# Kernel tuning notes

Measured on AMD Instinct MI355X. Metric: run time of the kernel, lower is better.

Reference implementation:

```python
import jax, jax.numpy as jnp
import numpy as np

N, D, YD, L = 500000, 256, 50, 1000


def setup_inputs() -> dict:
    key = jax.random.key(0)
    k_x, k_l, k_y, k_w1, k_w2 = jax.random.split(key, 5)
    lim1 = 1.0 / np.sqrt(D)
    return {
        "x": jax.random.normal(k_x, (N, D), dtype=jnp.float32),
        "labels": jax.random.randint(k_l, (N,), 0, L, dtype=jnp.int32),
        "y": jax.random.uniform(k_y, (N, YD), dtype=jnp.float32),
        "w1": jax.random.uniform(k_w1, (D, 1), jnp.float32, -lim1, lim1),
        "b1": jnp.zeros((1,), jnp.float32),
        "w2": jax.random.uniform(k_w2, (D, YD), jnp.float32, -lim1, lim1),
        "b2": jnp.zeros((YD,), jnp.float32),
        "num_labels": L,
    }


def reference(x, labels, y, w1, b1, w2, b2, num_labels):
    # sigmoid-gated features: a = sigmoid(x @ w1 + b1) * x   [N, D]
    a = jax.nn.sigmoid(x @ w1 + b1) * x
    # segment counts per label (labels assumed dense 0..L-1, all present)
    counts = jax.ops.segment_sum(jnp.ones((x.shape[0],), x.dtype), labels,
                                 num_segments=num_labels)
    denom = jnp.maximum(counts, 1.0)[:, None]  # guard empty segments
    # segment mean of gated features  [L, D]
    res = jax.ops.segment_sum(a, labels, num_segments=num_labels) / denom
    # softmax(linear2(res))  [L, YD]
    prediction = jax.nn.softmax(res @ w2 + b2, axis=1)
    # segment mean of soft targets  [L, YD]
    y_mean = jax.ops.segment_sum(y, labels, num_segments=num_labels) / denom
    # torch CrossEntropyLoss with probability targets applies log_softmax
    # to its input (here: already-softmaxed prediction) -- faithful double softmax
    logp = jax.nn.log_softmax(prediction, axis=1)
    return -jnp.mean(jnp.sum(y_mean * logp, axis=1))
```

## Files before the change

kernel.cpp:

```cpp
#include <hip/hip_runtime.h>
#include <math.h>

#define NROWS 500000
#define DIM 256
#define YDIM 50
#define NLAB 1000

#define XT 64
#define NTX ((NROWS + XT - 1) / XT)
#define XBLOCKS 256
#define ASTRIDE 264
#define ZC 51

#define YT 128
#define NTY ((NROWS + YT - 1) / YT)
#define YBLOCKS 256

typedef __attribute__((ext_vector_type(8))) short frag_ab;
typedef __attribute__((ext_vector_type(4))) float frag_cd;

__device__ __forceinline__ float b2f(unsigned short u) {
    return __uint_as_float(((unsigned)u) << 16);
}
__device__ __forceinline__ unsigned short f2b(float f) {
    unsigned u = __float_as_uint(f);
    return (unsigned short)((u + 0x7fffu + ((u >> 16) & 1u)) >> 16);
}
__device__ __forceinline__ unsigned cvt_pk_bf16(float lo, float hi) {
    unsigned r;
    asm("v_cvt_pk_bf16_f32 %0, %1, %2" : "=v"(r) : "v"(lo), "v"(hi));
    return r;
}
__device__ __forceinline__ void bar_lds() {
    asm volatile("s_waitcnt lgkmcnt(0)\n\ts_barrier" ::: "memory");
}

__global__ __launch_bounds__(1024) void k_xstream(
    const float* __restrict__ x, const int* __restrict__ labels,
    const float* __restrict__ w1, const float* __restrict__ b1,
    const float* __restrict__ w2, unsigned short* __restrict__ zpart,
    float* __restrict__ out)
{
    __shared__ __align__(16) unsigned short sA[XT * ASTRIDE];
    __shared__ __align__(16) float zst[XT][52];
    __shared__ __align__(16) unsigned short accz[NLAB * YDIM];
    __shared__ int slab[2][XT];

    const int tid = threadIdx.x, lane = tid & 63, wib = tid >> 6;
    const int bid = blockIdx.x;
    const int mh = wib >> 2, jt = wib & 3;

    if (bid == 0 && tid == 0) out[0] = 0.0f;
    for (int k = tid; k < NLAB * YDIM / 2; k += 1024)
        reinterpret_cast<unsigned*>(accz)[k] = 0u;

    frag_ab bfr[8];
    {
        const int n = 16 * jt + (lane & 15);
        #pragma unroll
        for (int s = 0; s < 8; ++s) {
            const int k0 = 32 * s + (lane >> 4) * 8;
            #pragma unroll
            for (int i = 0; i < 8; ++i) {
                const int kk = k0 + i;
                float v = 0.f;
                if (n < YDIM)       v = w2[kk * YDIM + n];
                else if (n == YDIM) v = w1[kk];
                bfr[s][i] = (short)f2b(v);
            }
        }
    }
    const float b1v = b1[0];
    __syncthreads();

    auto PREF = [&](int t, float4* r) {
        #pragma unroll
        for (int k = 0; k < 4; ++k) {
            const int rg = t * XT + 4 * wib + k;
            r[k] = (rg < NROWS)
                 ? reinterpret_cast<const float4*>(x)[(size_t)rg * 64 + lane]
                 : make_float4(0.f, 0.f, 0.f, 0.f);
        }
    };
    auto LLAB = [&](int t) -> int {
        const int rg = t * XT + tid;
        return (tid < XT && rg < NROWS) ? labels[rg] : 0;
    };

    auto process = [&](int pft, float4* r, int& lb, int par) {
        if (tid < XT) slab[par][tid] = lb;
        uint2 pk[4];
        #pragma unroll
        for (int k = 0; k < 4; ++k) {
            pk[k].x = cvt_pk_bf16(r[k].x, r[k].y);
            pk[k].y = cvt_pk_bf16(r[k].z, r[k].w);
        }
        PREF(pft, r);
        lb = LLAB(pft);
        const int row = 4 * wib;
        #pragma unroll
        for (int k = 0; k < 4; ++k)
            *reinterpret_cast<uint2*>(&sA[(row + k) * ASTRIDE + lane * 4]) = pk[k];
        bar_lds();

        frag_cd c = {0.f, 0.f, 0.f, 0.f};
        #pragma unroll
        for (int s = 0; s < 8; ++s) {
            frag_ab a = *reinterpret_cast<const frag_ab*>(
                &sA[(16 * mh + (lane & 15)) * ASTRIDE + 32 * s + (lane >> 4) * 8]);
            c = __builtin_amdgcn_mfma_f32_16x16x32_bf16(a, bfr[s], c, 0, 0, 0);
        }
        const int zr = 16 * mh + (lane >> 4) * 4;
        const int zc = 16 * jt + (lane & 15);
        if (zc < ZC) {
            zst[zr + 0][zc] = c[0]; zst[zr + 1][zc] = c[1];
            zst[zr + 2][zc] = c[2]; zst[zr + 3][zc] = c[3];
        }
        bar_lds();

        {
            const int lbl_lane = slab[par][lane];
            unsigned long long mask = __ballot((lbl_lane & 15) == wib);
            while (mask) {
                const int r2 = __builtin_ctzll(mask);
                mask &= mask - 1;
                const int lbv = __shfl(lbl_lane, r2);
                const float d = zst[r2][YDIM];
                const float g = 1.0f / (1.0f + __expf(-(d + b1v)));
                if (lane < 25) {
                    const float2 zv =
                        *reinterpret_cast<const float2*>(&zst[r2][2 * lane]);
                    unsigned* ap =
                        reinterpret_cast<unsigned*>(&accz[lbv * YDIM + 2 * lane]);
                    const unsigned old = *ap;
                    const float lo = b2f((unsigned short)(old & 0xffffu)) + g * zv.x;
                    const float hi = b2f((unsigned short)(old >> 16))     + g * zv.y;
                    *ap = cvt_pk_bf16(lo, hi);
                }
            }
        }
    };

    float4 rA[4], rB[4];
    PREF(bid, rA);
    PREF(bid + XBLOCKS, rB);
    int lbA = LLAB(bid), lbB = LLAB(bid + XBLOCKS);
    int par = 0;
    for (int t = bid; t < NTX; t += 2 * XBLOCKS) {
        process(t + 2 * XBLOCKS, rA, lbA, par); par ^= 1;
        if (t + XBLOCKS < NTX) {
            process(t + 3 * XBLOCKS, rB, lbB, par); par ^= 1;
        }
    }
    __syncthreads();
    unsigned short* zp = zpart + (size_t)bid * (NLAB * YDIM);
    for (int k = tid; k < NLAB * YDIM; k += 1024) zp[k] = accz[k];
}

__global__ __launch_bounds__(1024) void k_ystream(
    const float* __restrict__ y, const int* __restrict__ labels,
    unsigned short* __restrict__ ypart, int* __restrict__ gcnt)
{
    __shared__ __align__(16) unsigned short accy[NLAB * YDIM];
    __shared__ __align__(16) float yst[2][YT * YDIM];
    __shared__ int slab[2][YT];
    __shared__ int cnt[NLAB];

    const int tid = threadIdx.x, lane = tid & 63, wib = tid >> 6;
    const int bid = blockIdx.x;

    for (int k = tid; k < NLAB * YDIM / 2; k += 1024)
        reinterpret_cast<unsigned*>(accy)[k] = 0u;
    for (int k = tid; k < NLAB; k += 1024) cnt[k] = 0;
    __syncthreads();

    auto PREFY = [&](int t, float* v, int& myl) {
        const size_t base = (size_t)t * YT * YDIM;
        const int n = (t < NTY) ? (min(YT, NROWS - t * YT) * YDIM) : 0;
        #pragma unroll
        for (int i = 0; i < 7; ++i) {
            const int k = tid + i * 1024;
            v[i] = (k < n) ? y[base + k] : 0.f;
        }
        const int rg = t * YT + tid;
        myl = (tid < YT && t < NTY && rg < NROWS) ? labels[rg] : -1;
    };

    auto process = [&](int pft, float* v, int& myl, int par) {
        #pragma unroll
        for (int i = 0; i < 7; ++i) {
            const int k = tid + i * 1024;
            if (k < YT * YDIM) yst[par][k] = v[i];
        }
        if (tid < YT) {
            const bool valid = (myl >= 0);
            slab[par][tid] = valid ? myl : 0;
            if (valid) atomicAdd(&cnt[myl], 1);
        }
        PREFY(pft, v, myl);
        bar_lds();

        {
            const int l0 = slab[par][lane];
            const int l1 = slab[par][64 + lane];
            unsigned long long m0 = __ballot((l0 & 15) == wib);
            unsigned long long m1 = __ballot((l1 & 15) == wib);
            while (m0) {
                const int r = __builtin_ctzll(m0); m0 &= m0 - 1;
                const int lb = __shfl(l0, r);
                if (lane < 25) {
                    const float2 yv = *reinterpret_cast<const float2*>(
                        &yst[par][r * YDIM + 2 * lane]);
                    unsigned* ap =
                        reinterpret_cast<unsigned*>(&accy[lb * YDIM + 2 * lane]);
                    const unsigned old = *ap;
                    const float lo = b2f((unsigned short)(old & 0xffffu)) + yv.x;
                    const float hi = b2f((unsigned short)(old >> 16))     + yv.y;
                    *ap = cvt_pk_bf16(lo, hi);
                }
            }
            while (m1) {
                const int r = __builtin_ctzll(m1); m1 &= m1 - 1;
                const int lb = __shfl(l1, r);
                if (lane < 25) {
                    const float2 yv = *reinterpret_cast<const float2*>(
                        &yst[par][(64 + r) * YDIM + 2 * lane]);
                    unsigned* ap =
                        reinterpret_cast<unsigned*>(&accy[lb * YDIM + 2 * lane]);
                    const unsigned old = *ap;
                    const float lo = b2f((unsigned short)(old & 0xffffu)) + yv.x;
                    const float hi = b2f((unsigned short)(old >> 16))     + yv.y;
                    *ap = cvt_pk_bf16(lo, hi);
                }
            }
        }
    };

    float vA[7], vB[7];
    int mA, mB;
    PREFY(bid, vA, mA);
    PREFY(bid + YBLOCKS, vB, mB);
    int par = 0;
    for (int t = bid; t < NTY; t += 2 * YBLOCKS) {
        process(t + 2 * YBLOCKS, vA, mA, par); par ^= 1;
        if (t + YBLOCKS < NTY) {
            process(t + 3 * YBLOCKS, vB, mB, par); par ^= 1;
        }
    }
    __syncthreads();
    unsigned short* yp = ypart + (size_t)bid * (NLAB * YDIM);
    for (int k = tid; k < NLAB * YDIM; k += 1024) yp[k] = accy[k];
    for (int k = tid; k < NLAB; k += 1024)
        if (cnt[k]) atomicAdd(&gcnt[k], cnt[k]);
}

__global__ __launch_bounds__(256) void k_finalize(
    const unsigned short* __restrict__ zpart,
    const unsigned short* __restrict__ ypart,
    const int* __restrict__ gcnt,
    const float* __restrict__ b2, float* __restrict__ out)
{
    const int tid = threadIdx.x, lane = tid & 63, grp = tid >> 6;
    const int k0 = blockIdx.x * 200;

    float zs = 0.f, ys = 0.f;
    if (tid < 200) {
        const size_t idx = (size_t)k0 + tid;
        #pragma unroll 4
        for (int p = 0; p < XBLOCKS; ++p) {
            zs += b2f(zpart[(size_t)p * (NLAB * YDIM) + idx]);
            ys += b2f(ypart[(size_t)p * (NLAB * YDIM) + idx]);
        }
    }
    __shared__ float zl[200], yl[200];
    if (tid < 200) { zl[tid] = zs; yl[tid] = ys; }
    __syncthreads();

    const int l = blockIdx.x * 4 + grp;
    const bool act = lane < YDIM;
    const float zv = act ? zl[grp * 50 + lane] : 0.f;
    const float yv = act ? yl[grp * 50 + lane] : 0.f;

    const float denom = fmaxf((float)gcnt[l], 1.0f);
    const float NEG = -3.402823466e38f;
    float logit = act ? (zv / denom + b2[lane]) : NEG;
    const float ymean = act ? (yv / denom) : 0.f;

    float m = logit;
    #pragma unroll
    for (int o = 32; o > 0; o >>= 1) m = fmaxf(m, __shfl_xor(m, o));
    float e = act ? __expf(logit - m) : 0.f;
    float s = e;
    #pragma unroll
    for (int o = 32; o > 0; o >>= 1) s += __shfl_xor(s, o);
    const float p = e / s;

    float pm = act ? p : NEG;
    float m2 = pm;
    #pragma unroll
    for (int o = 32; o > 0; o >>= 1) m2 = fmaxf(m2, __shfl_xor(m2, o));
    float e2 = act ? __expf(p - m2) : 0.f;
    float s2 = e2;
    #pragma unroll
    for (int o = 32; o > 0; o >>= 1) s2 += __shfl_xor(s2, o);
    const float logp = p - m2 - __logf(s2);

    float contrib = act ? ymean * logp : 0.f;
    #pragma unroll
    for (int o = 32; o > 0; o >>= 1) contrib += __shfl_xor(contrib, o);
    if (lane == 0) atomicAdd(out, -contrib / (float)NLAB);
}

extern "C" void kernel_launch(void* const* d_in, const int* in_sizes, int n_in,
                              void* d_out, int out_size, void* d_ws, size_t ws_size,
                              hipStream_t stream) {
    const float* x      = (const float*)d_in[0];
    const int*   labels = (const int*)  d_in[1];
    const float* y      = (const float*)d_in[2];
    const float* w1     = (const float*)d_in[3];
    const float* b1     = (const float*)d_in[4];
    const float* w2     = (const float*)d_in[5];
    const float* b2     = (const float*)d_in[6];
    float* out = (float*)d_out;

    int* gcnt = (int*)d_ws;
    unsigned short* zpart = (unsigned short*)((char*)d_ws + 4096);
    unsigned short* ypart = (unsigned short*)((char*)d_ws + 4096 +
                             (size_t)XBLOCKS * NLAB * YDIM * 2);

    hipMemsetAsync(gcnt, 0, NLAB * sizeof(int), stream);
    k_xstream<<<XBLOCKS, 1024, 0, stream>>>(x, labels, w1, b1, w2, zpart, out);
    k_ystream<<<YBLOCKS, 1024, 0, stream>>>(y, labels, ypart, gcnt);
    k_finalize<<<250, 256, 0, stream>>>(zpart, ypart, gcnt, b2, out);
}
```

Baseline: 201.3 us.

## Double y tile rows and stage y in LDS as packed bf16

The y-streaming kernel now handles 256 rows per tile instead of 128. Each thread loads float2 pairs, and the pairs are converted to packed bf16 before being written to the double-buffered LDS stage. This halves the staging footprint so the larger tile still fits in LDS, and halves the number of tile iterations and barriers. The accumulate loop is generalized to four 64-row groups. The cost is that y values are rounded to bf16 before accumulation, which adds precision loss on top of the existing bf16 accumulator.

```diff
diff --git a/kernel.cpp b/kernel.cpp
--- a/kernel.cpp
+++ b/kernel.cpp
@@ -12,9 +12,10 @@
 #define ASTRIDE 264
 #define ZC 51
 
-#define YT 128
+#define YT 256
 #define NTY ((NROWS + YT - 1) / YT)
 #define YBLOCKS 256
+#define YSLOTS (YT * YDIM / 2)
 
 typedef __attribute__((ext_vector_type(8))) short frag_ab;
 typedef __attribute__((ext_vector_type(4))) float frag_cd;
@@ -162,7 +163,7 @@
     unsigned short* __restrict__ ypart, int* __restrict__ gcnt)
 {
     __shared__ __align__(16) unsigned short accy[NLAB * YDIM];
-    __shared__ __align__(16) float yst[2][YT * YDIM];
+    __shared__ __align__(16) unsigned yst[2][YSLOTS];
     __shared__ int slab[2][YT];
     __shared__ int cnt[NLAB];
 
@@ -174,23 +175,24 @@
     for (int k = tid; k < NLAB; k += 1024) cnt[k] = 0;
     __syncthreads();
 
-    auto PREFY = [&](int t, float* v, int& myl) {
-        const size_t base = (size_t)t * YT * YDIM;
-        const int n = (t < NTY) ? (min(YT, NROWS - t * YT) * YDIM) : 0;
+    auto PREFY = [&](int t, float2* v, int& myl) {
+        const float2* Y2 = reinterpret_cast<const float2*>(y);
+        const size_t base = (size_t)t * YSLOTS;
+        const int n = (t < NTY) ? (min(YT, NROWS - t * YT) * (YDIM / 2)) : 0;
         #pragma unroll
         for (int i = 0; i < 7; ++i) {
             const int k = tid + i * 1024;
-            v[i] = (k < n) ? y[base + k] : 0.f;
+            v[i] = (k < n) ? Y2[base + k] : make_float2(0.f, 0.f);
         }
         const int rg = t * YT + tid;
         myl = (tid < YT && t < NTY && rg < NROWS) ? labels[rg] : -1;
     };
 
-    auto process = [&](int pft, float* v, int& myl, int par) {
+    auto process = [&](int pft, float2* v, int& myl, int par) {
         #pragma unroll
         for (int i = 0; i < 7; ++i) {
             const int k = tid + i * 1024;
-            if (k < YT * YDIM) yst[par][k] = v[i];
+            if (k < YSLOTS) yst[par][k] = cvt_pk_bf16(v[i].x, v[i].y);
         }
         if (tid < YT) {
             const bool valid = (myl >= 0);
@@ -200,43 +202,29 @@
         PREFY(pft, v, myl);
         bar_lds();
 
-        {
-            const int l0 = slab[par][lane];
-            const int l1 = slab[par][64 + lane];
-            unsigned long long m0 = __ballot((l0 & 15) == wib);
-            unsigned long long m1 = __ballot((l1 & 15) == wib);
-            while (m0) {
-                const int r = __builtin_ctzll(m0); m0 &= m0 - 1;
-                const int lb = __shfl(l0, r);
+        #pragma unroll
+        for (int gq = 0; gq < 4; ++gq) {
+            const int lv = slab[par][64 * gq + lane];
+            unsigned long long m = __ballot((lv & 15) == wib);
+            while (m) {
+                const int r = __builtin_ctzll(m); m &= m - 1;
+                const int lb = __shfl(lv, r);
                 if (lane < 25) {
-                    const float2 yv = *reinterpret_cast<const float2*>(
-                        &yst[par][r * YDIM + 2 * lane]);
+                    const unsigned pkv = yst[par][(64 * gq + r) * 25 + lane];
                     unsigned* ap =
                         reinterpret_cast<unsigned*>(&accy[lb * YDIM + 2 * lane]);
                     const unsigned old = *ap;
-                    const float lo = b2f((unsigned short)(old & 0xffffu)) + yv.x;
-                    const float hi = b2f((unsigned short)(old >> 16))     + yv.y;
+                    const float lo = b2f((unsigned short)(old & 0xffffu)) +
+                                     b2f((unsigned short)(pkv & 0xffffu));
+                    const float hi = b2f((unsigned short)(old >> 16)) +
+                                     b2f((unsigned short)(pkv >> 16));
                     *ap = cvt_pk_bf16(lo, hi);
                 }
             }
-            while (m1) {
-                const int r = __builtin_ctzll(m1); m1 &= m1 - 1;
-                const int lb = __shfl(l1, r);
-                if (lane < 25) {
-                    const float2 yv = *reinterpret_cast<const float2*>(
-                        &yst[par][(64 + r) * YDIM + 2 * lane]);
-                    unsigned* ap =
-                        reinterpret_cast<unsigned*>(&accy[lb * YDIM + 2 * lane]);
-                    const unsigned old = *ap;
-                    const float lo = b2f((unsigned short)(old & 0xffffu)) + yv.x;
-                    const float hi = b2f((unsigned short)(old >> 16))     + yv.y;
-                    *ap = cvt_pk_bf16(lo, hi);
-                }
-            }
-        }
-    };
-
-    float vA[7], vB[7];
+        }
+    };
+
+    float2 vA[7], vB[7];
     int mA, mB;
     PREFY(bid, vA, mA);
     PREFY(bid + YBLOCKS, vB, mB);
```

Result: slower. 211.6 us (+5.2%).

## Load MFMA A-fragments directly from global memory, drop LDS staging

Applied to the files above, without the earlier changes.

Each lane now loads the x row segments it needs for its MFMA A-fragments straight from global memory and converts them to bf16 in registers. This removes the sA shared-memory staging buffer and one barrier per tile. zst is double-buffered by parity so the single remaining barrier is enough. Prefetch depth falls from two tiles to one, but each thread now holds sixteen float4 registers. Four waves (the jt dimension) each load the same rows, so global and cache traffic for x per tile grows, and the per-lane access pattern is less coalesced.

```diff
diff --git a/kernel.cpp b/kernel.cpp
--- a/kernel.cpp
+++ b/kernel.cpp
@@ -9,7 +9,6 @@
 #define XT 64
 #define NTX ((NROWS + XT - 1) / XT)
 #define XBLOCKS 256
-#define ASTRIDE 264
 #define ZC 51
 
 #define YT 128
@@ -41,8 +40,7 @@
     const float* __restrict__ w2, unsigned short* __restrict__ zpart,
     float* __restrict__ out)
 {
-    __shared__ __align__(16) unsigned short sA[XT * ASTRIDE];
-    __shared__ __align__(16) float zst[XT][52];
+    __shared__ __align__(16) float zst[2][XT][52];
     __shared__ __align__(16) unsigned short accz[NLAB * YDIM];
     __shared__ int slab[2][XT];
 
@@ -73,13 +71,18 @@
     const float b1v = b1[0];
     __syncthreads();
 
-    auto PREF = [&](int t, float4* r) {
-        #pragma unroll
-        for (int k = 0; k < 4; ++k) {
-            const int rg = t * XT + 4 * wib + k;
-            r[k] = (rg < NROWS)
-                 ? reinterpret_cast<const float4*>(x)[(size_t)rg * 64 + lane]
-                 : make_float4(0.f, 0.f, 0.f, 0.f);
+    const int arow = 16 * mh + (lane & 15);
+    const int kq   = (lane >> 4) * 2;
+
+    auto PREFA = [&](int t, float4* r) {
+        const int rg = t * XT + arow;
+        const bool ok = (t < NTX) && (rg < NROWS);
+        const float4* base = reinterpret_cast<const float4*>(x) + (size_t)rg * 64;
+        #pragma unroll
+        for (int s = 0; s < 8; ++s) {
+            const int fi = 8 * s + kq;
+            r[2 * s]     = ok ? base[fi]     : make_float4(0.f, 0.f, 0.f, 0.f);
+            r[2 * s + 1] = ok ? base[fi + 1] : make_float4(0.f, 0.f, 0.f, 0.f);
         }
     };
     auto LLAB = [&](int t) -> int {
@@ -89,32 +92,27 @@
 
     auto process = [&](int pft, float4* r, int& lb, int par) {
         if (tid < XT) slab[par][tid] = lb;
-        uint2 pk[4];
-        #pragma unroll
-        for (int k = 0; k < 4; ++k) {
-            pk[k].x = cvt_pk_bf16(r[k].x, r[k].y);
-            pk[k].y = cvt_pk_bf16(r[k].z, r[k].w);
-        }
-        PREF(pft, r);
+
+        frag_cd c = {0.f, 0.f, 0.f, 0.f};
+        #pragma unroll
+        for (int s = 0; s < 8; ++s) {
+            frag_ab a;
+            unsigned* au = reinterpret_cast<unsigned*>(&a);
+            au[0] = cvt_pk_bf16(r[2 * s].x,     r[2 * s].y);
+            au[1] = cvt_pk_bf16(r[2 * s].z,     r[2 * s].w);
+            au[2] = cvt_pk_bf16(r[2 * s + 1].x, r[2 * s + 1].y);
+            au[3] = cvt_pk_bf16(r[2 * s + 1].z, r[2 * s + 1].w);
+            c = __builtin_amdgcn_mfma_f32_16x16x32_bf16(a, bfr[s], c, 0, 0, 0);
+        }
+
+        PREFA(pft, r);
         lb = LLAB(pft);
-        const int row = 4 * wib;
-        #pragma unroll
-        for (int k = 0; k < 4; ++k)
-            *reinterpret_cast<uint2*>(&sA[(row + k) * ASTRIDE + lane * 4]) = pk[k];
-        bar_lds();
-
-        frag_cd c = {0.f, 0.f, 0.f, 0.f};
-        #pragma unroll
-        for (int s = 0; s < 8; ++s) {
-            frag_ab a = *reinterpret_cast<const frag_ab*>(
-                &sA[(16 * mh + (lane & 15)) * ASTRIDE + 32 * s + (lane >> 4) * 8]);
-            c = __builtin_amdgcn_mfma_f32_16x16x32_bf16(a, bfr[s], c, 0, 0, 0);
-        }
+
         const int zr = 16 * mh + (lane >> 4) * 4;
         const int zc = 16 * jt + (lane & 15);
         if (zc < ZC) {
-            zst[zr + 0][zc] = c[0]; zst[zr + 1][zc] = c[1];
-            zst[zr + 2][zc] = c[2]; zst[zr + 3][zc] = c[3];
+            zst[par][zr + 0][zc] = c[0]; zst[par][zr + 1][zc] = c[1];
+            zst[par][zr + 2][zc] = c[2]; zst[par][zr + 3][zc] = c[3];
         }
         bar_lds();
 
@@ -125,11 +123,11 @@
                 const int r2 = __builtin_ctzll(mask);
                 mask &= mask - 1;
                 const int lbv = __shfl(lbl_lane, r2);
-                const float d = zst[r2][YDIM];
+                const float d = zst[par][r2][YDIM];
                 const float g = 1.0f / (1.0f + __expf(-(d + b1v)));
                 if (lane < 25) {
                     const float2 zv =
-                        *reinterpret_cast<const float2*>(&zst[r2][2 * lane]);
+                        *reinterpret_cast<const float2*>(&zst[par][r2][2 * lane]);
                     unsigned* ap =
                         reinterpret_cast<unsigned*>(&accz[lbv * YDIM + 2 * lane]);
                     const unsigned old = *ap;
@@ -141,16 +139,13 @@
         }
     };
 
-    float4 rA[4], rB[4];
-    PREF(bid, rA);
-    PREF(bid + XBLOCKS, rB);
-    int lbA = LLAB(bid), lbB = LLAB(bid + XBLOCKS);
+    float4 r[16];
+    PREFA(bid, r);
+    int lb = LLAB(bid);
     int par = 0;
-    for (int t = bid; t < NTX; t += 2 * XBLOCKS) {
-        process(t + 2 * XBLOCKS, rA, lbA, par); par ^= 1;
-        if (t + XBLOCKS < NTX) {
-            process(t + 3 * XBLOCKS, rB, lbB, par); par ^= 1;
-        }
+    for (int t = bid; t < NTX; t += XBLOCKS) {
+        process(t + XBLOCKS, r, lb, par);
+        par ^= 1;
     }
     __syncthreads();
     unsigned short* zp = zpart + (size_t)bid * (NLAB * YDIM);
```

After: 334.6 us. +66.2%, slower.

## Split x-stream label accumulators across block pairs to halve LDS footprint

Applied to the files above, without the earlier changes.

The x-stream kernel now launches twice as many 512-thread blocks on 32-row tiles. The two blocks of each pair process the same tile, and each accumulates only the labels of one parity into a half-size bf16 LDS table. Finalize is updated to gather the z partials by parity. The smaller LDS and block size are meant to let more blocks reside per CU and overlap memory with the scatter work. The cost is that every x tile is loaded and multiplied twice, relying on L2 to absorb the duplicate read, and the per-tile barriers cover smaller tiles.

```diff
diff --git a/kernel.cpp b/kernel.cpp
--- a/kernel.cpp
+++ b/kernel.cpp
@@ -5,10 +5,12 @@
 #define DIM 256
 #define YDIM 50
 #define NLAB 1000
-
-#define XT 64
-#define NTX ((NROWS + XT - 1) / XT)
-#define XBLOCKS 256
+#define HLAB 500
+
+#define XT 32
+#define NTX (NROWS / XT)
+#define XBLOCKS 512
+#define XPAIRS 256
 #define ASTRIDE 264
 #define ZC 51
 
@@ -35,7 +37,7 @@
     asm volatile("s_waitcnt lgkmcnt(0)\n\ts_barrier" ::: "memory");
 }
 
-__global__ __launch_bounds__(1024) void k_xstream(
+__global__ __launch_bounds__(512, 4) void k_xstream(
     const float* __restrict__ x, const int* __restrict__ labels,
     const float* __restrict__ w1, const float* __restrict__ b1,
     const float* __restrict__ w2, unsigned short* __restrict__ zpart,
@@ -43,15 +45,17 @@
 {
     __shared__ __align__(16) unsigned short sA[XT * ASTRIDE];
     __shared__ __align__(16) float zst[XT][52];
-    __shared__ __align__(16) unsigned short accz[NLAB * YDIM];
+    __shared__ __align__(16) unsigned short accz[HLAB * YDIM];
     __shared__ int slab[2][XT];
 
     const int tid = threadIdx.x, lane = tid & 63, wib = tid >> 6;
     const int bid = blockIdx.x;
+    const int p   = bid & 1;
+    const int tb  = bid >> 1;
     const int mh = wib >> 2, jt = wib & 3;
 
     if (bid == 0 && tid == 0) out[0] = 0.0f;
-    for (int k = tid; k < NLAB * YDIM / 2; k += 1024)
+    for (int k = tid; k < HLAB * YDIM / 2; k += 512)
         reinterpret_cast<unsigned*>(accz)[k] = 0u;
 
     frag_ab bfr[8];
@@ -77,14 +81,14 @@
         #pragma unroll
         for (int k = 0; k < 4; ++k) {
             const int rg = t * XT + 4 * wib + k;
-            r[k] = (rg < NROWS)
+            r[k] = (t < NTX && rg < NROWS)
                  ? reinterpret_cast<const float4*>(x)[(size_t)rg * 64 + lane]
                  : make_float4(0.f, 0.f, 0.f, 0.f);
         }
     };
     auto LLAB = [&](int t) -> int {
         const int rg = t * XT + tid;
-        return (tid < XT && rg < NROWS) ? labels[rg] : 0;
+        return (tid < XT && t < NTX && rg < NROWS) ? labels[rg] : -1;
     };
 
     auto process = [&](int pft, float4* r, int& lb, int par) {
@@ -119,8 +123,11 @@
         bar_lds();
 
         {
-            const int lbl_lane = slab[par][lane];
-            unsigned long long mask = __ballot((lbl_lane & 15) == wib);
+            const int lbl_lane = slab[par][lane & 31];
+            const bool own = (lane < 32) && (lbl_lane >= 0) &&
+                             ((lbl_lane & 1) == p) &&
+                             (((lbl_lane >> 1) & 7) == wib);
+            unsigned long long mask = __ballot(own);
             while (mask) {
                 const int r2 = __builtin_ctzll(mask);
                 mask &= mask - 1;
@@ -130,8 +137,8 @@
                 if (lane < 25) {
                     const float2 zv =
                         *reinterpret_cast<const float2*>(&zst[r2][2 * lane]);
-                    unsigned* ap =
-                        reinterpret_cast<unsigned*>(&accz[lbv * YDIM + 2 * lane]);
+                    unsigned* ap = reinterpret_cast<unsigned*>(
+                        &accz[(lbv >> 1) * YDIM + 2 * lane]);
                     const unsigned old = *ap;
                     const float lo = b2f((unsigned short)(old & 0xffffu)) + g * zv.x;
                     const float hi = b2f((unsigned short)(old >> 16))     + g * zv.y;
@@ -142,19 +149,19 @@
     };
 
     float4 rA[4], rB[4];
-    PREF(bid, rA);
-    PREF(bid + XBLOCKS, rB);
-    int lbA = LLAB(bid), lbB = LLAB(bid + XBLOCKS);
+    PREF(tb, rA);
+    PREF(tb + XPAIRS, rB);
+    int lbA = LLAB(tb), lbB = LLAB(tb + XPAIRS);
     int par = 0;
-    for (int t = bid; t < NTX; t += 2 * XBLOCKS) {
-        process(t + 2 * XBLOCKS, rA, lbA, par); par ^= 1;
-        if (t + XBLOCKS < NTX) {
-            process(t + 3 * XBLOCKS, rB, lbB, par); par ^= 1;
+    for (int t = tb; t < NTX; t += 2 * XPAIRS) {
+        process(t + 2 * XPAIRS, rA, lbA, par); par ^= 1;
+        if (t + XPAIRS < NTX) {
+            process(t + 3 * XPAIRS, rB, lbB, par); par ^= 1;
         }
     }
     __syncthreads();
-    unsigned short* zp = zpart + (size_t)bid * (NLAB * YDIM);
-    for (int k = tid; k < NLAB * YDIM; k += 1024) zp[k] = accz[k];
+    unsigned short* zp = zpart + (size_t)bid * (HLAB * YDIM);
+    for (int k = tid; k < HLAB * YDIM; k += 512) zp[k] = accz[k];
 }
 
 __global__ __launch_bounds__(1024) void k_ystream(
@@ -265,12 +272,16 @@
 
     float zs = 0.f, ys = 0.f;
     if (tid < 200) {
-        const size_t idx = (size_t)k0 + tid;
+        const int flat = k0 + tid;
+        const int l = flat / 50, c = flat - 50 * l;
+        const int pp = l & 1;
+        const size_t zidx = (size_t)(l >> 1) * YDIM + c;
         #pragma unroll 4
-        for (int p = 0; p < XBLOCKS; ++p) {
-            zs += b2f(zpart[(size_t)p * (NLAB * YDIM) + idx]);
-            ys += b2f(ypart[(size_t)p * (NLAB * YDIM) + idx]);
-        }
+        for (int j = 0; j < XPAIRS; ++j)
+            zs += b2f(zpart[(size_t)(2 * j + pp) * (HLAB * YDIM) + zidx]);
+        #pragma unroll 4
+        for (int pb = 0; pb < YBLOCKS; ++pb)
+            ys += b2f(ypart[(size_t)pb * (NLAB * YDIM) + flat]);
     }
     __shared__ float zl[200], yl[200];
     if (tid < 200) { zl[tid] = zs; yl[tid] = ys; }
@@ -326,10 +337,10 @@
     int* gcnt = (int*)d_ws;
     unsigned short* zpart = (unsigned short*)((char*)d_ws + 4096);
     unsigned short* ypart = (unsigned short*)((char*)d_ws + 4096 +
-                             (size_t)XBLOCKS * NLAB * YDIM * 2);
+                             (size_t)XBLOCKS * HLAB * YDIM * 2);
 
     hipMemsetAsync(gcnt, 0, NLAB * sizeof(int), stream);
-    k_xstream<<<XBLOCKS, 1024, 0, stream>>>(x, labels, w1, b1, w2, zpart, out);
+    k_xstream<<<XBLOCKS, 512, 0, stream>>>(x, labels, w1, b1, w2, zpart, out);
     k_ystream<<<YBLOCKS, 1024, 0, stream>>>(y, labels, ypart, gcnt);
     k_finalize<<<250, 256, 0, stream>>>(zpart, ypart, gcnt, b2, out);
 }
```

Result: slower. 282.1 us (+40.1%).
